# Kernel optimization log

Hardware: AMD Instinct MI355X
Metric: run time of the kernel (lower is better)

Reference implementation:

```python
import jax, jax.numpy as jnp
import numpy as np

D = 2048
HQ = 32
HKV = 8
DH = D // HQ          # 64
GROUP = HQ // HKV     # 4
B, T = 2, 2048


def setup_inputs() -> dict:
    key = jax.random.key(0)
    ks = jax.random.split(key, 5)
    s = 0.02
    return {
        "x": jax.random.normal(ks[0], (B, T, D), dtype=jnp.float32),
        "Wq": jax.random.normal(ks[1], (D, D), dtype=jnp.float32) * s,
        "Wk": jax.random.normal(ks[2], (D, HKV * DH), dtype=jnp.float32) * s,
        "Wv": jax.random.normal(ks[3], (D, HKV * DH), dtype=jnp.float32) * s,
        "Wo": jax.random.normal(ks[4], (D, D), dtype=jnp.float32) * s,
    }


def reference(x, Wq, Wk, Wv, Wo):
    Bsz, Tlen, _ = x.shape
    # projections
    q = (x @ Wq).reshape(Bsz, Tlen, HQ, DH).transpose(0, 2, 1, 3)    # [B,hq,T,dh]
    k = (x @ Wk).reshape(Bsz, Tlen, HKV, DH).transpose(0, 2, 1, 3)   # [B,hkv,T,dh]
    v = (x @ Wv).reshape(Bsz, Tlen, HKV, DH).transpose(0, 2, 1, 3)
    # GQA: repeat each kv head GROUP times along the head dim
    k = jnp.repeat(k, GROUP, axis=1)                                  # [B,hq,T,dh]
    v = jnp.repeat(v, GROUP, axis=1)
    scale = 1.0 / jnp.sqrt(jnp.asarray(DH, dtype=x.dtype))
    att = jnp.einsum("bhqd,bhkd->bhqk", q, k) * scale                # [B,hq,T,T]
    p = jax.nn.softmax(att, axis=-1)
    out = jnp.einsum("bhqk,bhkd->bhqd", p, v)                        # [B,hq,T,dh]
    out = out.transpose(0, 2, 1, 3).reshape(Bsz, Tlen, D)            # [B,T,D]
    return out @ Wo
```

## Files before the change

kernel.cpp:

```cpp
#include <hip/hip_runtime.h>
#include <stdint.h>

typedef __bf16 bf16;
typedef __bf16 bf16x8 __attribute__((ext_vector_type(8)));
typedef __bf16 bf16x4_t __attribute__((ext_vector_type(4)));
typedef float f32x4 __attribute__((ext_vector_type(4)));

#define HQ_N 32
#define DH_N 64
#define SEQ 2048
#define NTOK 4096

#if __has_builtin(__builtin_amdgcn_exp2f)
#define EXP2(x) __builtin_amdgcn_exp2f(x)
#else
#define EXP2(x) __expf((x) * 0.69314718056f)
#endif

#define QSCALE 0.18033688011112042f

__device__ __forceinline__ void async_ld16(const bf16* g, bf16* l) {
    __builtin_amdgcn_global_load_lds(
        (__attribute__((address_space(1))) void*)(uintptr_t)(g),
        (__attribute__((address_space(3))) void*)(uint32_t)(uintptr_t)(l),
        16, 0, 0);
}

__global__ __launch_bounds__(256) void k_cast_bf16(const float* __restrict__ in,
                                                   bf16* __restrict__ out, int n4) {
    int i = blockIdx.x * 256 + threadIdx.x;
    if (i < n4) {
        float4 f = ((const float4*)in)[i];
        bf16x4_t v = {(bf16)f.x, (bf16)f.y, (bf16)f.z, (bf16)f.w};
        ((bf16x4_t*)out)[i] = v;
    }
}

__global__ __launch_bounds__(256) void k_cast_transpose(const float* __restrict__ in,
                                                        bf16* __restrict__ out,
                                                        int R, int C) {
    __shared__ float t[32][33];
    int c0 = blockIdx.x * 32, r0 = blockIdx.y * 32;
    int tx = threadIdx.x, ty = threadIdx.y;
    for (int i = ty; i < 32; i += 8)
        t[i][tx] = in[(size_t)(r0 + i) * C + c0 + tx];
    __syncthreads();
    for (int i = ty; i < 32; i += 8)
        out[(size_t)(c0 + i) * R + r0 + tx] = (bf16)t[tx][i];
}

__global__ __launch_bounds__(256) void k_gemm(
    const bf16* __restrict__ A, const bf16* __restrict__ BT,
    int lda, int ldb, int M, int N, int K, int mode,
    float* __restrict__ Cf, int ldc,
    bf16* __restrict__ Qb, bf16* __restrict__ Kb, bf16* __restrict__ VTb)
{
    __shared__ bf16 As[128 * 32];
    __shared__ bf16 Bs[128 * 32];
    const int tid  = threadIdx.x;
    const int lane = tid & 63;
    const int w    = tid >> 6;
    const int l15  = lane & 15, quad = lane >> 4;
    const int wm = (w >> 1) * 64, wn = (w & 1) * 64;
    const int mb = M >> 7;
    const int band_sz = mb * 8;
    const int band = blockIdx.x / band_sz;
    const int rsr  = blockIdx.x % band_sz;
    const int mi = rsr >> 3, ni = band * 8 + (rsr & 7);

    const bf16* Ab = A + (size_t)mi * 128 * lda;
    const bf16* Bb = BT + (size_t)ni * 128 * ldb;

    f32x4 acc[4][4] = {};

    for (int k0 = 0; k0 < K; k0 += 32) {
        __syncthreads();
#pragma unroll
        for (int c = 0; c < 2; ++c) {
            int i = tid + c * 256;
            int row = i >> 2, kc = i & 3;
            async_ld16(Ab + (size_t)row * lda + k0 + kc * 8, &As[i * 8]);
            async_ld16(Bb + (size_t)row * ldb + k0 + kc * 8, &Bs[i * 8]);
        }
        __syncthreads();
        bf16x8 af[4], bfr[4];
#pragma unroll
        for (int mt = 0; mt < 4; ++mt)
            af[mt] = *(const bf16x8*)(As + (wm + mt * 16 + l15) * 32 + quad * 8);
#pragma unroll
        for (int nt = 0; nt < 4; ++nt)
            bfr[nt] = *(const bf16x8*)(Bs + (wn + nt * 16 + l15) * 32 + quad * 8);
#pragma unroll
        for (int mt = 0; mt < 4; ++mt)
#pragma unroll
            for (int nt = 0; nt < 4; ++nt)
                acc[mt][nt] = __builtin_amdgcn_mfma_f32_16x16x32_bf16(
                    af[mt], bfr[nt], acc[mt][nt], 0, 0, 0);
    }

#pragma unroll
    for (int mt = 0; mt < 4; ++mt) {
#pragma unroll
        for (int nt = 0; nt < 4; ++nt) {
            int rg0 = mi * 128 + wm + mt * 16 + quad * 4;
            int cg  = ni * 128 + wn + nt * 16 + l15;
#pragma unroll
            for (int r = 0; r < 4; ++r) {
                float v = acc[mt][nt][r];
                int rg = rg0 + r;
                if (mode == 2) {
                    Cf[(size_t)rg * ldc + cg] = v;
                } else {
                    if (cg < 2048)      Qb[(size_t)rg * 2048 + cg] = (bf16)(v * QSCALE);
                    else if (cg < 2560) Kb[(size_t)rg * 512 + (cg - 2048)] = (bf16)v;
                    else                VTb[(size_t)(cg - 2560) * NTOK + rg] = (bf16)v;
                }
            }
        }
    }
}

__global__ __launch_bounds__(256, 2) void k_attn(
    const bf16* __restrict__ Qb,
    const bf16* __restrict__ Kb,
    const bf16* __restrict__ VTb,
    bf16* __restrict__ Ob)
{
    __shared__ bf16 Ks[64 * 64];
    __shared__ bf16 Vt[64 * 64];
    __shared__ bf16 Ps[256 * 64];
    __shared__ float Ls[256];

    const int tid  = threadIdx.x;
    const int lane = tid & 63;
    const int w    = tid >> 6;
    const int l15  = lane & 15, quad = lane >> 4;
    const int l7   = l15 & 7;

    const int bid = blockIdx.x;
    const int qt  = bid & 7;
    const int hq  = (bid >> 3) & 31;
    const int b   = bid >> 8;
    const int hkv = hq >> 2;
    const int q0  = qt * 256;
    const int wq0 = w * 64;
    const size_t tokbase = (size_t)b * SEQ;

    bf16* Pw = Ps + w * (64 * 64);

    bf16x8 qf[4][2];
#pragma unroll
    for (int nt = 0; nt < 4; ++nt)
#pragma unroll
        for (int ks = 0; ks < 2; ++ks)
            qf[nt][ks] = *(const bf16x8*)(
                Qb + (tokbase + q0 + wq0 + nt * 16 + l15) * 2048 + hq * DH_N + ks * 32 + quad * 8);

    f32x4 acc_o[4][4] = {};
    float lsum[4] = {0.f, 0.f, 0.f, 0.f};

    for (int kt = 0; kt < 32; ++kt) {
        const int k0 = kt * 64;
        __syncthreads();
#pragma unroll
        for (int c = 0; c < 2; ++c) {
            int i = tid + c * 256;
            int row = i >> 3, c8 = i & 7;
            int dst = row * 64 + 8 * (c8 ^ (row & 7));
            uint4 kv = *(const uint4*)(Kb + (tokbase + k0 + row) * 512 + hkv * DH_N + c8 * 8);
            *(uint4*)&Ks[dst] = kv;
            uint4 vv = *(const uint4*)(VTb + ((size_t)hkv * DH_N + row) * NTOK + tokbase + k0 + c8 * 8);
            *(uint4*)&Vt[dst] = vv;
        }
        __syncthreads();

        f32x4 accs[4][4] = {};
#pragma unroll
        for (int ks = 0; ks < 2; ++ks) {
            const int ch = 8 * ((ks * 4 + quad) ^ l7);
            bf16x8 kf[4];
#pragma unroll
            for (int mt = 0; mt < 4; ++mt)
                kf[mt] = *(const bf16x8*)(Ks + (mt * 16 + l15) * 64 + ch);
#pragma unroll
            for (int mt = 0; mt < 4; ++mt)
#pragma unroll
                for (int nt = 0; nt < 4; ++nt)
                    accs[mt][nt] = __builtin_amdgcn_mfma_f32_16x16x32_bf16(
                        kf[mt], qf[nt][ks], accs[mt][nt], 0, 0, 0);
        }

#pragma unroll
        for (int mt = 0; mt < 4; ++mt) {
            const int wch = (mt * 2 + (quad >> 1));
            const int sub = (quad & 1) * 4;
#pragma unroll
            for (int nt = 0; nt < 4; ++nt) {
                float p0 = EXP2(accs[mt][nt][0]);
                float p1 = EXP2(accs[mt][nt][1]);
                float p2 = EXP2(accs[mt][nt][2]);
                float p3 = EXP2(accs[mt][nt][3]);
                lsum[nt] += (p0 + p1) + (p2 + p3);
                bf16x4_t pv = {(bf16)p0, (bf16)p1, (bf16)p2, (bf16)p3};
                *(bf16x4_t*)&Pw[(nt * 16 + l15) * 64 + 8 * (wch ^ l7) + sub] = pv;
            }
        }

#pragma unroll
        for (int ks = 0; ks < 2; ++ks) {
            const int ch = 8 * ((ks * 4 + quad) ^ l7);
            bf16x8 pf[4], vf[4];
#pragma unroll
            for (int mt = 0; mt < 4; ++mt)
                pf[mt] = *(const bf16x8*)(Pw + (mt * 16 + l15) * 64 + ch);
#pragma unroll
            for (int nt = 0; nt < 4; ++nt)
                vf[nt] = *(const bf16x8*)(Vt + (nt * 16 + l15) * 64 + ch);
#pragma unroll
            for (int mt = 0; mt < 4; ++mt)
#pragma unroll
                for (int nt = 0; nt < 4; ++nt)
                    acc_o[mt][nt] = __builtin_amdgcn_mfma_f32_16x16x32_bf16(
                        pf[mt], vf[nt], acc_o[mt][nt], 0, 0, 0);
        }
    }

#pragma unroll
    for (int nt = 0; nt < 4; ++nt) {
        float s = lsum[nt];
        s += __shfl_xor(s, 16);
        s += __shfl_xor(s, 32);
        Ls[w * 64 + nt * 16 + l15] = 1.0f / s;
    }

#pragma unroll
    for (int mt = 0; mt < 4; ++mt) {
#pragma unroll
        for (int r = 0; r < 4; ++r) {
            float rl = Ls[w * 64 + mt * 16 + quad * 4 + r];
            int qrow = q0 + wq0 + mt * 16 + quad * 4 + r;
#pragma unroll
            for (int nt = 0; nt < 4; ++nt) {
                float v = acc_o[mt][nt][r] * rl;
                Ob[(tokbase + qrow) * 2048 + hq * DH_N + nt * 16 + l15] = (bf16)v;
            }
        }
    }
}

extern "C" void kernel_launch(void* const* d_in, const int* in_sizes, int n_in,
                              void* d_out, int out_size, void* d_ws, size_t ws_size,
                              hipStream_t stream)
{
    const float* x  = (const float*)d_in[0];
    const float* Wq = (const float*)d_in[1];
    const float* Wk = (const float*)d_in[2];
    const float* Wv = (const float*)d_in[3];
    const float* Wo = (const float*)d_in[4];
    float* out = (float*)d_out;

    bf16* ws    = (bf16*)d_ws;
    bf16* xb    = ws;
    bf16* WqkvT = xb    + (size_t)4096 * 2048;
    bf16* WoT   = WqkvT + (size_t)3072 * 2048;
    bf16* Qb    = WoT   + (size_t)2048 * 2048;
    bf16* Kb    = Qb    + (size_t)4096 * 2048;
    bf16* VTb   = Kb    + (size_t)4096 * 512;
    bf16* Ob    = VTb   + (size_t)512 * 4096;

    dim3 tb(32, 8);
    k_cast_bf16<<<8192, 256, 0, stream>>>(x, xb, 4096 * 2048 / 4);
    k_cast_transpose<<<dim3(64, 64), tb, 0, stream>>>(Wq, WqkvT, 2048, 2048);
    k_cast_transpose<<<dim3(16, 64), tb, 0, stream>>>(Wk, WqkvT + (size_t)2048 * 2048, 2048, 512);
    k_cast_transpose<<<dim3(16, 64), tb, 0, stream>>>(Wv, WqkvT + (size_t)2560 * 2048, 2048, 512);
    k_cast_transpose<<<dim3(64, 64), tb, 0, stream>>>(Wo, WoT, 2048, 2048);

    k_gemm<<<(4096 / 128) * (3072 / 128), 256, 0, stream>>>(
        xb, WqkvT, 2048, 2048, 4096, 3072, 2048, 1,
        nullptr, 0, Qb, Kb, VTb);

    k_attn<<<512, 256, 0, stream>>>(Qb, Kb, VTb, Ob);

    k_gemm<<<(4096 / 128) * (2048 / 128), 256, 0, stream>>>(
        Ob, WoT, 2048, 2048, 4096, 2048, 2048, 2,
        out, 2048, nullptr, nullptr, nullptr);
}
```

Measured before the change: 347.0 us.

## Widen GEMM K-tile with swizzled LDS, async attention loads, coalesced V^T epilogue

The GEMM K-step grows from 32 to 64 with an XOR-swizzled LDS layout to avoid bank conflicts, and gets launch bounds of 3 blocks per CU. The QKV epilogue now branches per block instead of per element, and the V^T output is staged through LDS so its strided stores become coalesced 16-byte writes. The attention kernel switches K/V tile loads to async global-to-LDS copies with pointer increments, and the cast-transpose kernel uses 64x64 tiles with float4 reads and bf16x4 writes. These target LDS conflicts, uncoalesced stores and load-issue overhead, at the cost of larger shared memory per GEMM block and extra syncs in the V epilogue.

```diff
diff --git a/kernel.cpp b/kernel.cpp
--- a/kernel.cpp
+++ b/kernel.cpp
@@ -39,83 +39,138 @@
 __global__ __launch_bounds__(256) void k_cast_transpose(const float* __restrict__ in,
                                                         bf16* __restrict__ out,
                                                         int R, int C) {
-    __shared__ float t[32][33];
-    int c0 = blockIdx.x * 32, r0 = blockIdx.y * 32;
-    int tx = threadIdx.x, ty = threadIdx.y;
-    for (int i = ty; i < 32; i += 8)
-        t[i][tx] = in[(size_t)(r0 + i) * C + c0 + tx];
+    __shared__ float t[64][65];
+    const int tid = threadIdx.x;
+    const int c0 = blockIdx.x * 64, r0 = blockIdx.y * 64;
+#pragma unroll
+    for (int c = 0; c < 4; ++c) {
+        int i = tid + c * 256;
+        int row = i >> 4, cc = (i & 15) * 4;
+        float4 v = *(const float4*)(in + (size_t)(r0 + row) * C + c0 + cc);
+        t[row][cc + 0] = v.x; t[row][cc + 1] = v.y;
+        t[row][cc + 2] = v.z; t[row][cc + 3] = v.w;
+    }
     __syncthreads();
-    for (int i = ty; i < 32; i += 8)
-        out[(size_t)(c0 + i) * R + r0 + tx] = (bf16)t[tx][i];
-}
-
-__global__ __launch_bounds__(256) void k_gemm(
+#pragma unroll
+    for (int c = 0; c < 4; ++c) {
+        int i = tid + c * 256;
+        int row = i >> 4, cc = (i & 15) * 4;
+        bf16x4_t v = {(bf16)t[cc + 0][row], (bf16)t[cc + 1][row],
+                      (bf16)t[cc + 2][row], (bf16)t[cc + 3][row]};
+        *(bf16x4_t*)(out + (size_t)(c0 + row) * R + r0 + cc) = v;
+    }
+}
+
+__global__ __launch_bounds__(256, 3) void k_gemm(
     const bf16* __restrict__ A, const bf16* __restrict__ BT,
     int lda, int ldb, int M, int N, int K, int mode,
     float* __restrict__ Cf, int ldc,
     bf16* __restrict__ Qb, bf16* __restrict__ Kb, bf16* __restrict__ VTb)
 {
-    __shared__ bf16 As[128 * 32];
-    __shared__ bf16 Bs[128 * 32];
+    __shared__ bf16 S[16384];
+    bf16* As = S;
+    bf16* Bs = S + 8192;
+
     const int tid  = threadIdx.x;
     const int lane = tid & 63;
     const int w    = tid >> 6;
     const int l15  = lane & 15, quad = lane >> 4;
+    const int l7   = l15 & 7;
     const int wm = (w >> 1) * 64, wn = (w & 1) * 64;
+
     const int mb = M >> 7;
-    const int band_sz = mb * 8;
-    const int band = blockIdx.x / band_sz;
-    const int rsr  = blockIdx.x % band_sz;
+    const int band = blockIdx.x / (mb * 8);
+    const int rsr  = blockIdx.x % (mb * 8);
     const int mi = rsr >> 3, ni = band * 8 + (rsr & 7);
 
-    const bf16* Ab = A + (size_t)mi * 128 * lda;
-    const bf16* Bb = BT + (size_t)ni * 128 * ldb;
+    const int srow = tid >> 3;
+    const int sc8e = ((tid & 7) ^ (srow & 7)) * 8;
+    const bf16* aP = A  + (size_t)(mi * 128 + srow) * lda + sc8e;
+    const bf16* bP = BT + (size_t)(ni * 128 + srow) * ldb + sc8e;
 
     f32x4 acc[4][4] = {};
 
-    for (int k0 = 0; k0 < K; k0 += 32) {
-        __syncthreads();
-#pragma unroll
-        for (int c = 0; c < 2; ++c) {
+    for (int k0 = 0; k0 < K; k0 += 64) {
+        __syncthreads();
+#pragma unroll
+        for (int c = 0; c < 4; ++c) {
+            async_ld16(aP + (size_t)c * 32 * lda, &As[(tid + c * 256) * 8]);
+            async_ld16(bP + (size_t)c * 32 * ldb, &Bs[(tid + c * 256) * 8]);
+        }
+        aP += 64; bP += 64;
+        __syncthreads();
+#pragma unroll
+        for (int ks = 0; ks < 2; ++ks) {
+            const int ch = 8 * (((ks << 2) | quad) ^ l7);
+            bf16x8 af[4], bfr[4];
+#pragma unroll
+            for (int mt = 0; mt < 4; ++mt)
+                af[mt] = *(const bf16x8*)(As + (wm + mt * 16 + l15) * 64 + ch);
+#pragma unroll
+            for (int nt = 0; nt < 4; ++nt)
+                bfr[nt] = *(const bf16x8*)(Bs + (wn + nt * 16 + l15) * 64 + ch);
+#pragma unroll
+            for (int mt = 0; mt < 4; ++mt)
+#pragma unroll
+                for (int nt = 0; nt < 4; ++nt)
+                    acc[mt][nt] = __builtin_amdgcn_mfma_f32_16x16x32_bf16(
+                        af[mt], bfr[nt], acc[mt][nt], 0, 0, 0);
+        }
+    }
+
+    if (mode == 2) {
+#pragma unroll
+        for (int mt = 0; mt < 4; ++mt)
+#pragma unroll
+            for (int nt = 0; nt < 4; ++nt) {
+                int rg0 = mi * 128 + wm + mt * 16 + quad * 4;
+                int cg  = ni * 128 + wn + nt * 16 + l15;
+#pragma unroll
+                for (int r = 0; r < 4; ++r)
+                    Cf[(size_t)(rg0 + r) * ldc + cg] = acc[mt][nt][r];
+            }
+    } else if (ni < 16) {
+#pragma unroll
+        for (int mt = 0; mt < 4; ++mt)
+#pragma unroll
+            for (int nt = 0; nt < 4; ++nt) {
+                int rg0 = mi * 128 + wm + mt * 16 + quad * 4;
+                int cg  = ni * 128 + wn + nt * 16 + l15;
+#pragma unroll
+                for (int r = 0; r < 4; ++r)
+                    Qb[(size_t)(rg0 + r) * 2048 + cg] = (bf16)(acc[mt][nt][r] * QSCALE);
+            }
+    } else if (ni < 20) {
+#pragma unroll
+        for (int mt = 0; mt < 4; ++mt)
+#pragma unroll
+            for (int nt = 0; nt < 4; ++nt) {
+                int rg0 = mi * 128 + wm + mt * 16 + quad * 4;
+                int cg  = ni * 128 + wn + nt * 16 + l15 - 2048;
+#pragma unroll
+                for (int r = 0; r < 4; ++r)
+                    Kb[(size_t)(rg0 + r) * 512 + cg] = (bf16)acc[mt][nt][r];
+            }
+    } else {
+        __syncthreads();
+#pragma unroll
+        for (int mt = 0; mt < 4; ++mt)
+#pragma unroll
+            for (int nt = 0; nt < 4; ++nt) {
+                int rl0 = wm + mt * 16 + quad * 4;
+                int cl  = wn + nt * 16 + l15;
+#pragma unroll
+                for (int r = 0; r < 4; ++r)
+                    S[cl * 128 + rl0 + r] = (bf16)acc[mt][nt][r];
+            }
+        __syncthreads();
+        const int v0 = ni * 128 - 2560;
+#pragma unroll
+        for (int c = 0; c < 8; ++c) {
             int i = tid + c * 256;
-            int row = i >> 2, kc = i & 3;
-            async_ld16(Ab + (size_t)row * lda + k0 + kc * 8, &As[i * 8]);
-            async_ld16(Bb + (size_t)row * ldb + k0 + kc * 8, &Bs[i * 8]);
-        }
-        __syncthreads();
-        bf16x8 af[4], bfr[4];
-#pragma unroll
-        for (int mt = 0; mt < 4; ++mt)
-            af[mt] = *(const bf16x8*)(As + (wm + mt * 16 + l15) * 32 + quad * 8);
-#pragma unroll
-        for (int nt = 0; nt < 4; ++nt)
-            bfr[nt] = *(const bf16x8*)(Bs + (wn + nt * 16 + l15) * 32 + quad * 8);
-#pragma unroll
-        for (int mt = 0; mt < 4; ++mt)
-#pragma unroll
-            for (int nt = 0; nt < 4; ++nt)
-                acc[mt][nt] = __builtin_amdgcn_mfma_f32_16x16x32_bf16(
-                    af[mt], bfr[nt], acc[mt][nt], 0, 0, 0);
-    }
-
-#pragma unroll
-    for (int mt = 0; mt < 4; ++mt) {
-#pragma unroll
-        for (int nt = 0; nt < 4; ++nt) {
-            int rg0 = mi * 128 + wm + mt * 16 + quad * 4;
-            int cg  = ni * 128 + wn + nt * 16 + l15;
-#pragma unroll
-            for (int r = 0; r < 4; ++r) {
-                float v = acc[mt][nt][r];
-                int rg = rg0 + r;
-                if (mode == 2) {
-                    Cf[(size_t)rg * ldc + cg] = v;
-                } else {
-                    if (cg < 2048)      Qb[(size_t)rg * 2048 + cg] = (bf16)(v * QSCALE);
-                    else if (cg < 2560) Kb[(size_t)rg * 512 + (cg - 2048)] = (bf16)v;
-                    else                VTb[(size_t)(cg - 2560) * NTOK + rg] = (bf16)v;
-                }
-            }
+            int row = i >> 4, c8 = (i & 15) * 8;
+            uint4 vv = *(const uint4*)(S + row * 128 + c8);
+            *(uint4*)(VTb + (size_t)(v0 + row) * NTOK + mi * 128 + c8) = vv;
         }
     }
 }
@@ -148,6 +203,11 @@
 
     bf16* Pw = Ps + w * (64 * 64);
 
+    const int srow = tid >> 3;
+    const int sc8e = ((tid & 7) ^ (srow & 7)) * 8;
+    const bf16* kP = Kb  + (tokbase + srow) * 512 + hkv * DH_N + sc8e;
+    const bf16* vP = VTb + ((size_t)hkv * DH_N + srow) * NTOK + tokbase + sc8e;
+
     bf16x8 qf[4][2];
 #pragma unroll
     for (int nt = 0; nt < 4; ++nt)
@@ -160,24 +220,20 @@
     float lsum[4] = {0.f, 0.f, 0.f, 0.f};
 
     for (int kt = 0; kt < 32; ++kt) {
-        const int k0 = kt * 64;
         __syncthreads();
 #pragma unroll
         for (int c = 0; c < 2; ++c) {
-            int i = tid + c * 256;
-            int row = i >> 3, c8 = i & 7;
-            int dst = row * 64 + 8 * (c8 ^ (row & 7));
-            uint4 kv = *(const uint4*)(Kb + (tokbase + k0 + row) * 512 + hkv * DH_N + c8 * 8);
-            *(uint4*)&Ks[dst] = kv;
-            uint4 vv = *(const uint4*)(VTb + ((size_t)hkv * DH_N + row) * NTOK + tokbase + k0 + c8 * 8);
-            *(uint4*)&Vt[dst] = vv;
-        }
+            async_ld16(kP + (size_t)c * 32 * 512,  &Ks[(tid + c * 256) * 8]);
+            async_ld16(vP + (size_t)c * 32 * NTOK, &Vt[(tid + c * 256) * 8]);
+        }
+        kP += 64 * 512;
+        vP += 64;
         __syncthreads();
 
         f32x4 accs[4][4] = {};
 #pragma unroll
         for (int ks = 0; ks < 2; ++ks) {
-            const int ch = 8 * ((ks * 4 + quad) ^ l7);
+            const int ch = 8 * (((ks << 2) | quad) ^ l7);
             bf16x8 kf[4];
 #pragma unroll
             for (int mt = 0; mt < 4; ++mt)
@@ -208,7 +264,7 @@
 
 #pragma unroll
         for (int ks = 0; ks < 2; ++ks) {
-            const int ch = 8 * ((ks * 4 + quad) ^ l7);
+            const int ch = 8 * (((ks << 2) | quad) ^ l7);
             bf16x8 pf[4], vf[4];
 #pragma unroll
             for (int mt = 0; mt < 4; ++mt)
@@ -268,12 +324,11 @@
     bf16* VTb   = Kb    + (size_t)4096 * 512;
     bf16* Ob    = VTb   + (size_t)512 * 4096;
 
-    dim3 tb(32, 8);
     k_cast_bf16<<<8192, 256, 0, stream>>>(x, xb, 4096 * 2048 / 4);
-    k_cast_transpose<<<dim3(64, 64), tb, 0, stream>>>(Wq, WqkvT, 2048, 2048);
-    k_cast_transpose<<<dim3(16, 64), tb, 0, stream>>>(Wk, WqkvT + (size_t)2048 * 2048, 2048, 512);
-    k_cast_transpose<<<dim3(16, 64), tb, 0, stream>>>(Wv, WqkvT + (size_t)2560 * 2048, 2048, 512);
-    k_cast_transpose<<<dim3(64, 64), tb, 0, stream>>>(Wo, WoT, 2048, 2048);
+    k_cast_transpose<<<dim3(32, 32), 256, 0, stream>>>(Wq, WqkvT, 2048, 2048);
+    k_cast_transpose<<<dim3(8, 32), 256, 0, stream>>>(Wk, WqkvT + (size_t)2048 * 2048, 2048, 512);
+    k_cast_transpose<<<dim3(8, 32), 256, 0, stream>>>(Wv, WqkvT + (size_t)2560 * 2048, 2048, 512);
+    k_cast_transpose<<<dim3(32, 32), 256, 0, stream>>>(Wo, WoT, 2048, 2048);
 
     k_gemm<<<(4096 / 128) * (3072 / 128), 256, 0, stream>>>(
         xb, WqkvT, 2048, 2048, 4096, 3072, 2048, 1,
```

After: 302.0 us. 1.15x faster.
